# Kernel optimization log

Hardware: AMD Instinct MI355X
Metric: run time of the kernel (lower is better)

The kernel has to match this reference:

```python
import jax, jax.numpy as jnp
import numpy as np

N = 100000
E = 1600000
C = 192      # in_channels
GH = 256     # grapher hidden
FH = 512     # ffn hidden
EPS = 1e-5


def _bn(x, gamma, beta):
    # BatchNorm1d, training-mode batch statistics over the node axis
    mean = jnp.mean(x, axis=0)
    var = jnp.var(x, axis=0)
    return (x - mean) * jax.lax.rsqrt(var + EPS) * gamma + beta


def setup_inputs() -> dict:
    key = jax.random.key(0)
    ks = jax.random.split(key, 12)
    s = 0.02
    inp = {
        "x": jax.random.normal(ks[0], (N, C), dtype=jnp.float32),
        "edge_index": jax.random.randint(ks[1], (2, E), 0, N, dtype=jnp.int64),
        # Grapher fc1
        "Wg1": jax.random.normal(ks[2], (C, GH), jnp.float32) * s,
        "bg1": jnp.zeros((GH,), jnp.float32),
        "gg1": jnp.ones((GH,), jnp.float32),
        "beg1": jnp.zeros((GH,), jnp.float32),
        # GraphConv (lin_rel has bias, lin_root no bias, per PyG)
        "Wrel": jax.random.normal(ks[3], (GH, GH), jnp.float32) * s,
        "brel": jnp.zeros((GH,), jnp.float32),
        "Wroot": jax.random.normal(ks[4], (GH, GH), jnp.float32) * s,
        # Grapher fc2
        "Wg2": jax.random.normal(ks[5], (GH, C), jnp.float32) * s,
        "bg2": jnp.zeros((C,), jnp.float32),
        "gg2": jnp.ones((C,), jnp.float32),
        "beg2": jnp.zeros((C,), jnp.float32),
        # FFN fc1
        "Wf1": jax.random.normal(ks[6], (C, FH), jnp.float32) * s,
        "bf1": jnp.zeros((FH,), jnp.float32),
        "gf1": jnp.ones((FH,), jnp.float32),
        "bef1": jnp.zeros((FH,), jnp.float32),
        # FFN fc2
        "Wf2": jax.random.normal(ks[7], (FH, C), jnp.float32) * s,
        "bf2": jnp.zeros((C,), jnp.float32),
        "gf2": jnp.ones((C,), jnp.float32),
        "bef2": jnp.zeros((C,), jnp.float32),
    }
    return inp


def reference(x, edge_index, Wg1, bg1, gg1, beg1, Wrel, brel, Wroot,
              Wg2, bg2, gg2, beg2, Wf1, bf1, gf1, bef1, Wf2, bf2, gf2, bef2):
    n = x.shape[0]
    src, dst = edge_index[0], edge_index[1]

    # ---- Grapher ----
    shortcut = x
    h = _bn(x @ Wg1 + bg1, gg1, beg1)                       # [N, GH]
    # GraphConv: sum-aggregate neighbor messages at target nodes
    agg = jax.ops.segment_sum(h[src], dst, num_segments=n)  # [N, GH]
    gc = agg @ Wrel + brel + h @ Wroot
    h = jax.nn.gelu(gc, approximate=False)
    h = _bn(h @ Wg2 + bg2, gg2, beg2)                       # [N, C]
    x = h + shortcut

    # ---- FFN ----
    shortcut = x
    h = jax.nn.gelu(_bn(x @ Wf1 + bf1, gf1, bef1), approximate=False)
    h = _bn(h @ Wf2 + bf2, gf2, bef2)
    return h + shortcut
```

## Files before the change

kernel.cpp:

```cpp
#include <hip/hip_runtime.h>
#include <math.h>

typedef __bf16 bf16x8 __attribute__((ext_vector_type(8)));
typedef float  floatx4 __attribute__((ext_vector_type(4)));

__device__ inline float bf_lo(unsigned u){ return __uint_as_float(u << 16); }
__device__ inline float bf_hi(unsigned u){ return __uint_as_float(u & 0xffff0000u); }
__device__ inline unsigned short f2bf_u(float f){
    unsigned u = __float_as_uint(f);
    return (unsigned short)((u + 0x7fffu + ((u >> 16) & 1u)) >> 16);
}
__device__ inline unsigned pack2(float a, float b){
    return (unsigned)f2bf_u(a) | ((unsigned)f2bf_u(b) << 16);
}
__device__ inline float gelu_f(float v){
    return 0.5f * v * (1.f + erff(v * 0.70710678118654752f));
}
__device__ inline void gload_lds16(const void* g, void* l){
    __builtin_amdgcn_global_load_lds(
        (const __attribute__((address_space(1))) unsigned int*)g,
        (__attribute__((address_space(3))) unsigned int*)l, 16, 0, 0);
}

__global__ void zero_k(int* __restrict__ p, int n){
    int i = blockIdx.x * 256 + threadIdx.x;
    if (i < n) p[i] = 0;
}

__global__ void xcast_k(const float* __restrict__ x, unsigned short* __restrict__ xb, long n8){
    long i = (long)blockIdx.x * 256 + threadIdx.x;
    if (i < n8){
        const float4* p = (const float4*)(x + i * 8);
        float4 a = p[0], b = p[1];
        uint4 o;
        o.x = pack2(a.x, a.y); o.y = pack2(a.z, a.w);
        o.z = pack2(b.x, b.y); o.w = pack2(b.z, b.w);
        *(uint4*)(xb + i * 8) = o;
    }
}

__global__ void wprep_k(const float* __restrict__ W, unsigned short* __restrict__ Wt,
                        int K, int Ncols, int ostride, int ooffs){
    int idx = blockIdx.x * 256 + threadIdx.x;
    if (idx < K * Ncols){
        int k = idx / Ncols, n = idx - k * Ncols;
        Wt[(size_t)n * ostride + ooffs + k] = f2bf_u(W[idx]);
    }
}

__global__ void mkbn_k(const float* __restrict__ gsum, const float* __restrict__ gsq,
                       const float* __restrict__ gamma, const float* __restrict__ beta,
                       const float* __restrict__ brel,
                       float* __restrict__ scv, float* __restrict__ shv,
                       float* __restrict__ bias2, float* __restrict__ rvec,
                       int C_, float invN){
    int c = blockIdx.x * 256 + threadIdx.x;
    if (c < C_){
        float mean = gsum[c] * invN;
        float var  = gsq[c] * invN - mean * mean;
        float sc   = gamma[c] * rsqrtf(var + 1e-5f);
        scv[c] = sc;
        shv[c] = beta[c] - mean * sc;
        bias2[c] = brel[c];
        rvec[c]  = 0.f;
    }
}

__global__ void wscale_k(unsigned short* __restrict__ wt, const float* __restrict__ scv, int total){
    int i = blockIdx.x * 256 + threadIdx.x;
    if (i < total){
        float v = __uint_as_float(((unsigned)wt[i]) << 16);
        wt[i] = f2bf_u(v * scv[i & 255]);
    }
}

__global__ void biasrr_k(const float* __restrict__ Wrel, const float* __restrict__ Wroot,
                         const float* __restrict__ shv,
                         float* __restrict__ bias2, float* __restrict__ rvec){
    int m = threadIdx.x;
    int k0 = blockIdx.x * 32;
    float b2 = 0.f, rv = 0.f;
    for (int k = k0; k < k0 + 32; ++k){
        float s = shv[k];
        rv = fmaf(s, Wrel[k * 256 + m], rv);
        b2 = fmaf(s, Wroot[k * 256 + m], b2);
    }
    atomicAdd(&bias2[m], b2);
    atomicAdd(&rvec[m],  rv);
}

#define RBSH 9
#define RB   512
#define PCH  8192

__global__ __launch_bounds__(256)
void bhist_k(const int* __restrict__ dst, int* __restrict__ bcnt, int E){
    __shared__ int h[256];
    for (int i = threadIdx.x; i < 256; i += 256) h[i] = 0;
    __syncthreads();
    for (long i = (long)blockIdx.x * 256 + threadIdx.x; i < E; i += (long)gridDim.x * 256)
        atomicAdd(&h[dst[i] >> RBSH], 1);
    __syncthreads();
    int v = h[threadIdx.x];
    if (v) atomicAdd(&bcnt[threadIdx.x * 16], v);
}

__global__ void bscan_k(const int* __restrict__ bcnt, int* __restrict__ bbase,
                        int* __restrict__ bcur, int nbuk, int E){
    __shared__ int s[256];
    const int t = threadIdx.x;
    int v = (t < nbuk) ? bcnt[t * 16] : 0;
    s[t] = v; __syncthreads();
    for (int d = 1; d < 256; d <<= 1){
        int tt = (t >= d) ? s[t - d] : 0;
        __syncthreads();
        s[t] += tt;
        __syncthreads();
    }
    int excl = s[t] - v;
    if (t < nbuk){ bbase[t] = excl; bcur[t * 16] = excl; }
    if (t == 0) bbase[nbuk] = E;
}

__global__ __launch_bounds__(512)
void bpart_k(const int* __restrict__ src, const int* __restrict__ dst,
             int* __restrict__ bcur, int2* __restrict__ pairs, int E){
    __shared__ int h[256];
    __shared__ int s[256];
    __shared__ int cur[256];
    const int t = threadIdx.x;
    const int base = blockIdx.x * PCH;
    const int cnt = min(PCH, E - base);
    if (t < 256) h[t] = 0;
    __syncthreads();
    for (int i = t; i < cnt; i += 512)
        atomicAdd(&h[dst[base + i] >> RBSH], 1);
    __syncthreads();
    if (t < 256) s[t] = h[t];
    __syncthreads();
    for (int d = 1; d < 256; d <<= 1){
        int tt = 0;
        if (t < 256 && t >= d) tt = s[t - d];
        __syncthreads();
        if (t < 256) s[t] += tt;
        __syncthreads();
    }
    if (t < 256){
        int myc = h[t];
        int g = 0;
        if (myc) g = atomicAdd(&bcur[t * 16], myc);
        cur[t] = g;
    }
    __syncthreads();
    for (int i = t; i < cnt; i += 512){
        int d = dst[base + i];
        int b = d >> RBSH;
        int r = atomicAdd(&cur[b], 1);
        pairs[r] = make_int2(src[base + i], d);
    }
}

__global__ __launch_bounds__(1024)
void bbuild_k(const int2* __restrict__ pairs, const int* __restrict__ bbase,
              int* __restrict__ offsets, int* __restrict__ esrc, int N, int E){
    __shared__ int h[RB];
    __shared__ int s[RB];
    const int b = blockIdx.x;
    const int t = threadIdx.x;
    const int p0 = bbase[b], p1 = bbase[b + 1];
    if (t < RB) h[t] = 0;
    __syncthreads();
    for (int i = p0 + t; i < p1; i += 1024)
        atomicAdd(&h[pairs[i].y & (RB - 1)], 1);
    __syncthreads();
    int v = 0;
    if (t < RB){ v = h[t]; s[t] = v; }
    __syncthreads();
    for (int d = 1; d < RB; d <<= 1){
        int tt = 0;
        if (t < RB && t >= d) tt = s[t - d];
        __syncthreads();
        if (t < RB) s[t] += tt;
        __syncthreads();
    }
    if (t < RB){
        int node = (b << RBSH) + t;
        int excl = p0 + s[t] - v;
        if (node < N) offsets[node] = excl;
        h[t] = excl;
    }
    __syncthreads();
    for (int i = p0 + t; i < p1; i += 1024){
        int2 pr = pairs[i];
        int r = atomicAdd(&h[pr.y & (RB - 1)], 1);
        esrc[r] = pr.x;
    }
    if (b == 0 && t == 0) offsets[N] = E;
}

__global__ __launch_bounds__(256)
void agg_k(const unsigned short* __restrict__ hbn, const int* __restrict__ offsets,
           const int* __restrict__ esrc, unsigned short* __restrict__ aggout, int N){
    const int lane = threadIdx.x & 63;
    const int node = blockIdx.x * 4 + (threadIdx.x >> 6);
    if (node >= N) return;
    const int off  = offsets[node];
    const int end  = offsets[node + 1];
    const int half = lane >> 5;
    const int l32  = lane & 31;
    float a[8];
#pragma unroll
    for (int j = 0; j < 8; ++j) a[j] = 0.f;
    const unsigned short* hb = hbn + l32 * 8;
    for (int c = off; c < end; c += 64){
        const int e = c + lane;
        int sl = (e < end) ? esrc[e] : 0;
        const int cnt = min(64, end - c);
        for (int j = 0; j < cnt; j += 16){
            int   s[8];
            float m[8];
            uint4 u[8];
#pragma unroll
            for (int k = 0; k < 8; ++k){
                const int idx = j + 2 * k + half;
                s[k] = __shfl(sl, idx);
                m[k] = (idx < cnt) ? 1.f : 0.f;
            }
#pragma unroll
            for (int k = 0; k < 8; ++k)
                u[k] = *(const uint4*)(hb + (size_t)s[k] * 512);
#pragma unroll
            for (int k = 0; k < 8; ++k){
                a[0] = fmaf(m[k], bf_lo(u[k].x), a[0]);
                a[1] = fmaf(m[k], bf_hi(u[k].x), a[1]);
                a[2] = fmaf(m[k], bf_lo(u[k].y), a[2]);
                a[3] = fmaf(m[k], bf_hi(u[k].y), a[3]);
                a[4] = fmaf(m[k], bf_lo(u[k].z), a[4]);
                a[5] = fmaf(m[k], bf_hi(u[k].z), a[5]);
                a[6] = fmaf(m[k], bf_lo(u[k].w), a[6]);
                a[7] = fmaf(m[k], bf_hi(u[k].w), a[7]);
            }
        }
    }
#pragma unroll
    for (int j = 0; j < 8; ++j)
        a[j] += __shfl_xor(a[j], 32);
    if (half == 0){
        uint4 o;
        o.x = pack2(a[0], a[1]); o.y = pack2(a[2], a[3]);
        o.z = pack2(a[4], a[5]); o.w = pack2(a[6], a[7]);
        *(uint4*)(aggout + (size_t)node * 512 + l32 * 8) = o;
    }
}

template<int K, bool GELU_OUT, bool DEGBIAS, bool STATS>
__global__ __launch_bounds__(256)
void gemm3_k(const unsigned short* __restrict__ A, const unsigned short* __restrict__ Bt,
             const float* __restrict__ bias, unsigned short* __restrict__ Cp,
             long M, int NY, int ostride, int ooffs,
             const int* __restrict__ offs, const float* __restrict__ rvec,
             float* __restrict__ psum, float* __restrict__ psq){
    __shared__ unsigned short Xs[128 * 64];
    __shared__ unsigned short Ws[64 * 64];
    const int t    = threadIdx.x;
    const int lane = t & 63;
    const int w    = t >> 6;
    const int r16  = lane & 15;
    const int q4   = lane >> 4;

    const int nwg  = gridDim.x;
    const int orig = blockIdx.x;
    const int qq   = nwg >> 3, rr = nwg & 7;
    const int xcd  = orig & 7, kk = orig >> 3;
    const int wgid = (xcd < rr ? xcd * (qq + 1) : rr * (qq + 1) + (xcd - rr) * qq) + kk;
    const int xb   = wgid / NY;
    const int yb   = wgid - xb * NY;
    const long mbase = (long)xb * 128;
    const int  cb    = yb * 64;

    floatx4 acc[4][2];
#pragma unroll
    for (int ai = 0; ai < 4; ++ai)
#pragma unroll
        for (int bi = 0; bi < 2; ++bi) acc[ai][bi] = (floatx4)0.f;

    const int lrow = w * 8 + (lane >> 3);
    const int lk   = (lane & 7) * 8;
    const unsigned short* ga = A  + (size_t)(mbase + lrow) * K + lk;
    const unsigned short* gb = Bt + (size_t)(cb + lrow) * K + lk;
    unsigned short* lx = Xs + w * 512 + lane * 8;
    unsigned short* lw = Ws + w * 512 + lane * 8;

    for (int kt = 0; kt < K; kt += 64){
#pragma unroll
        for (int i = 0; i < 4; ++i)
            gload_lds16(ga + (size_t)i * 32 * K + kt, lx + i * 2048);
#pragma unroll
        for (int j = 0; j < 2; ++j)
            gload_lds16(gb + (size_t)j * 32 * K + kt, lw + j * 2048);
        asm volatile("s_waitcnt vmcnt(0)" ::: "memory");
        __syncthreads();
#pragma unroll
        for (int kc = 0; kc < 64; kc += 32){
            bf16x8 wf[4], xf[2];
#pragma unroll
            for (int ai = 0; ai < 4; ++ai)
                wf[ai] = *(const bf16x8*)(Ws + (ai * 16 + r16) * 64 + kc + q4 * 8);
#pragma unroll
            for (int bi = 0; bi < 2; ++bi)
                xf[bi] = *(const bf16x8*)(Xs + (w * 32 + bi * 16 + r16) * 64 + kc + q4 * 8);
#pragma unroll
            for (int ai = 0; ai < 4; ++ai)
#pragma unroll
                for (int bi = 0; bi < 2; ++bi)
                    acc[ai][bi] = __builtin_amdgcn_mfma_f32_16x16x32_bf16(
                        wf[ai], xf[bi], acc[ai][bi], 0, 0, 0);
        }
        __syncthreads();
    }

    float4 bv[4];
#pragma unroll
    for (int ai = 0; ai < 4; ++ai)
        bv[ai] = *(const float4*)(bias + cb + ai * 16 + q4 * 4);
    float4 rv[4];
    if constexpr (DEGBIAS){
#pragma unroll
        for (int ai = 0; ai < 4; ++ai)
            rv[ai] = *(const float4*)(rvec + cb + ai * 16 + q4 * 4);
    }
    float cs[4][4], cq[4][4];
    if constexpr (STATS){
#pragma unroll
        for (int ai = 0; ai < 4; ++ai)
#pragma unroll
            for (int j = 0; j < 4; ++j){ cs[ai][j] = 0.f; cq[ai][j] = 0.f; }
    }
#pragma unroll
    for (int bi = 0; bi < 2; ++bi){
        long node = mbase + w * 32 + bi * 16 + r16;
        const bool valid = node < M;
        float degf = 0.f;
        if constexpr (DEGBIAS){
            if (valid) degf = (float)(offs[node + 1] - offs[node]);
        }
        unsigned short* cp = Cp + (size_t)node * ostride + ooffs + cb;
#pragma unroll
        for (int ai = 0; ai < 4; ++ai){
            float v0 = acc[ai][bi][0] + bv[ai].x;
            float v1 = acc[ai][bi][1] + bv[ai].y;
            float v2 = acc[ai][bi][2] + bv[ai].z;
            float v3 = acc[ai][bi][3] + bv[ai].w;
            if constexpr (DEGBIAS){
                v0 = fmaf(degf, rv[ai].x, v0);
                v1 = fmaf(degf, rv[ai].y, v1);
                v2 = fmaf(degf, rv[ai].z, v2);
                v3 = fmaf(degf, rv[ai].w, v3);
            }
            if constexpr (STATS){
                float mm = valid ? 1.f : 0.f;
                cs[ai][0] += mm * v0; cq[ai][0] = fmaf(mm * v0, v0, cq[ai][0]);
                cs[ai][1] += mm * v1; cq[ai][1] = fmaf(mm * v1, v1, cq[ai][1]);
                cs[ai][2] += mm * v2; cq[ai][2] = fmaf(mm * v2, v2, cq[ai][2]);
                cs[ai][3] += mm * v3; cq[ai][3] = fmaf(mm * v3, v3, cq[ai][3]);
            }
            if constexpr (GELU_OUT){
                v0 = gelu_f(v0); v1 = gelu_f(v1); v2 = gelu_f(v2); v3 = gelu_f(v3);
            }
            if (valid){
                uint2 o; o.x = pack2(v0, v1); o.y = pack2(v2, v3);
                *(uint2*)(cp + ai * 16 + q4 * 4) = o;
            }
        }
    }

    if constexpr (STATS){
#pragma unroll
        for (int ai = 0; ai < 4; ++ai)
#pragma unroll
            for (int j = 0; j < 4; ++j){
#pragma unroll
                for (int m = 1; m < 16; m <<= 1){
                    cs[ai][j] += __shfl_xor(cs[ai][j], m);
                    cq[ai][j] += __shfl_xor(cq[ai][j], m);
                }
            }
        float* ssum = (float*)Xs;
        float* ssq  = ssum + 256;
        if (r16 == 0){
#pragma unroll
            for (int ai = 0; ai < 4; ++ai)
#pragma unroll
                for (int j = 0; j < 4; ++j){
                    ssum[w * 64 + ai * 16 + q4 * 4 + j] = cs[ai][j];
                    ssq [w * 64 + ai * 16 + q4 * 4 + j] = cq[ai][j];
                }
        }
        __syncthreads();
        if (t < 64){
            float s = 0.f, q = 0.f;
#pragma unroll
            for (int ww = 0; ww < 4; ++ww){ s += ssum[ww * 64 + t]; q += ssq[ww * 64 + t]; }
            const int nc = NY * 64;
            psum[(size_t)xb * nc + cb + t] = s;
            psq [(size_t)xb * nc + cb + t] = q;
        }
    }
}

__global__ void colreduce_k(const float* __restrict__ ps, const float* __restrict__ pq,
                            float* __restrict__ gsum, float* __restrict__ gsq,
                            int ncols, int nxb){
    __shared__ float ss[256], sq_[256];
    const int c = blockIdx.x;
    float s = 0.f, q = 0.f;
    for (int i = threadIdx.x; i < nxb; i += 256){
        s += ps[(size_t)i * ncols + c];
        q += pq[(size_t)i * ncols + c];
    }
    ss[threadIdx.x] = s; sq_[threadIdx.x] = q;
    __syncthreads();
    for (int d = 128; d > 0; d >>= 1){
        if (threadIdx.x < d){
            ss[threadIdx.x]  += ss[threadIdx.x + d];
            sq_[threadIdx.x] += sq_[threadIdx.x + d];
        }
        __syncthreads();
    }
    if (threadIdx.x == 0){ gsum[c] = ss[0]; gsq[c] = sq_[0]; }
}

template<int NCOLS, bool GELU_OUT, bool RES, bool RES_F32, bool OUT_F32>
__global__ __launch_bounds__(256)
void bn_apply_k(const unsigned short* __restrict__ in, void* __restrict__ outv,
                const void* __restrict__ resv,
                const float* __restrict__ gsum, const float* __restrict__ gsq,
                const float* __restrict__ gamma, const float* __restrict__ beta,
                long nrows, int ostride, int ooffs, float invN){
    __shared__ float s_scale[NCOLS], s_shift[NCOLS];
    for (int c = threadIdx.x; c < NCOLS; c += 256){
        float mean = gsum[c] * invN;
        float var  = gsq[c] * invN - mean * mean;
        float sc   = gamma[c] * rsqrtf(var + 1e-5f);
        s_scale[c] = sc;
        s_shift[c] = beta[c] - mean * sc;
    }
    __syncthreads();
    long i8 = ((long)blockIdx.x * 256 + threadIdx.x) * 8;
    if (i8 >= nrows * (long)NCOLS) return;
    long row  = i8 / NCOLS;
    int  col0 = (int)(i8 - row * NCOLS);
    uint4 u = *(const uint4*)(in + i8);
    float v[8];
    v[0] = bf_lo(u.x); v[1] = bf_hi(u.x); v[2] = bf_lo(u.y); v[3] = bf_hi(u.y);
    v[4] = bf_lo(u.z); v[5] = bf_hi(u.z); v[6] = bf_lo(u.w); v[7] = bf_hi(u.w);
#pragma unroll
    for (int j = 0; j < 8; ++j){
        v[j] = v[j] * s_scale[col0 + j] + s_shift[col0 + j];
        if constexpr (GELU_OUT) v[j] = gelu_f(v[j]);
    }
    if constexpr (RES){
        if constexpr (RES_F32){
            const float4* rp = (const float4*)((const float*)resv + i8);
            float4 r0 = rp[0], r1 = rp[1];
            v[0] += r0.x; v[1] += r0.y; v[2] += r0.z; v[3] += r0.w;
            v[4] += r1.x; v[5] += r1.y; v[6] += r1.z; v[7] += r1.w;
        } else {
            uint4 r = *(const uint4*)((const unsigned short*)resv + i8);
            v[0] += bf_lo(r.x); v[1] += bf_hi(r.x); v[2] += bf_lo(r.y); v[3] += bf_hi(r.y);
            v[4] += bf_lo(r.z); v[5] += bf_hi(r.z); v[6] += bf_lo(r.w); v[7] += bf_hi(r.w);
        }
    }
    long opos = row * ostride + ooffs + col0;
    if constexpr (OUT_F32){
        float4* op = (float4*)((float*)outv + opos);
        op[0] = make_float4(v[0], v[1], v[2], v[3]);
        op[1] = make_float4(v[4], v[5], v[6], v[7]);
    } else {
        uint4 o;
        o.x = pack2(v[0], v[1]); o.y = pack2(v[2], v[3]);
        o.z = pack2(v[4], v[5]); o.w = pack2(v[6], v[7]);
        *(uint4*)((unsigned short*)outv + opos) = o;
    }
}

extern "C" void kernel_launch(void* const* d_in, const int* in_sizes, int n_in,
                              void* d_out, int out_size, void* d_ws, size_t ws_size,
                              hipStream_t stream){
    const int C = 192, GH = 256, FH = 512;
    const float* x    = (const float*)d_in[0];
    const int*   ei   = (const int*)d_in[1];
    const float* Wg1  = (const float*)d_in[2];
    const float* bg1  = (const float*)d_in[3];
    const float* gg1  = (const float*)d_in[4];
    const float* beg1 = (const float*)d_in[5];
    const float* Wrel = (const float*)d_in[6];
    const float* brel = (const float*)d_in[7];
    const float* Wroot= (const float*)d_in[8];
    const float* Wg2  = (const float*)d_in[9];
    const float* bg2  = (const float*)d_in[10];
    const float* gg2  = (const float*)d_in[11];
    const float* beg2 = (const float*)d_in[12];
    const float* Wf1  = (const float*)d_in[13];
    const float* bf1  = (const float*)d_in[14];
    const float* gf1  = (const float*)d_in[15];
    const float* bef1 = (const float*)d_in[16];
    const float* Wf2  = (const float*)d_in[17];
    const float* bf2  = (const float*)d_in[18];
    const float* gf2  = (const float*)d_in[19];
    const float* bef2 = (const float*)d_in[20];

    const int N = in_sizes[0] / C;
    const int E = in_sizes[1] / 2;
    const int* e_src = ei;
    const int* e_dst = ei + E;

    char* wp = (char*)d_ws;
    auto carve = [&](size_t bytes) -> void* {
        void* p = (void*)wp; wp += (bytes + 255) & ~(size_t)255; return p;
    };
    unsigned short* wt_g1 = (unsigned short*)carve((size_t)GH * C * 2);
    unsigned short* wt_rr = (unsigned short*)carve((size_t)GH * 512 * 2);
    unsigned short* wt_g2 = (unsigned short*)carve((size_t)C * GH * 2);
    unsigned short* wt_f1 = (unsigned short*)carve((size_t)FH * C * 2);
    unsigned short* wt_f2 = (unsigned short*)carve((size_t)C * FH * 2);
    float* stats = (float*)carve(2 * (size_t)(GH + C + FH + C) * 4);
    float* sum1 = stats;        float* sq1 = sum1 + GH;
    float* sum2 = sq1 + GH;     float* sq2 = sum2 + C;
    float* sum3 = sq2 + C;      float* sq3 = sum3 + FH;
    float* sum4 = sq3 + FH;     float* sq4 = sum4 + C;
    float* scv   = (float*)carve(256 * 4);
    float* shv   = (float*)carve(256 * 4);
    float* bias2 = (float*)carve(256 * 4);
    float* rvec  = (float*)carve(256 * 4);
    const int GB = (N + 127) / 128;
    float* psum = (float*)carve((size_t)GB * 512 * 4);
    float* psq  = (float*)carve((size_t)GB * 512 * 4);
    unsigned short* buf0  = (unsigned short*)carve((size_t)N * 512 * 2);
    unsigned short* bufAG = (unsigned short*)carve((size_t)N * 512 * 2);
    int* offsets = (int*)carve((size_t)(N + 1) * 4);
    int* esrc    = (int*)carve((size_t)E * 4);
    int* bcnt    = (int*)carve((size_t)256 * 16 * 4);
    int* bbase   = (int*)carve((size_t)257 * 4);
    int* bcur    = (int*)carve((size_t)256 * 16 * 4);
    int2* pairs = (int2*)buf0;
    unsigned short* x_bf = buf0;
    unsigned short* g    = buf0;
    unsigned short* f1   = buf0;
    unsigned short* AG   = bufAG;
    unsigned short* h2   = bufAG;
    unsigned short* h4   = bufAG + (size_t)N * C;
    (void)ws_size; (void)n_in; (void)out_size;

    const float invN = 1.0f / (float)N;
    const int nbuk = (N + RB - 1) >> RBSH;

    wprep_k<<<(C * GH + 255) / 256, 256, 0, stream>>>(Wg1, wt_g1, C, GH, C, 0);
    wprep_k<<<(GH * GH + 255) / 256, 256, 0, stream>>>(Wrel, wt_rr, GH, GH, 512, 0);
    wprep_k<<<(GH * GH + 255) / 256, 256, 0, stream>>>(Wroot, wt_rr, GH, GH, 512, GH);
    wprep_k<<<(GH * C + 255) / 256, 256, 0, stream>>>(Wg2, wt_g2, GH, C, GH, 0);
    wprep_k<<<(C * FH + 255) / 256, 256, 0, stream>>>(Wf1, wt_f1, C, FH, C, 0);
    wprep_k<<<(FH * C + 255) / 256, 256, 0, stream>>>(Wf2, wt_f2, FH, C, FH, 0);

    zero_k<<<(256 * 16 + 255) / 256, 256, 0, stream>>>(bcnt, 256 * 16);

    bhist_k<<<1024, 256, 0, stream>>>(e_dst, bcnt, E);
    bscan_k<<<1, 256, 0, stream>>>(bcnt, bbase, bcur, nbuk, E);
    bpart_k<<<(E + PCH - 1) / PCH, 512, 0, stream>>>(e_src, e_dst, bcur, pairs, E);
    bbuild_k<<<nbuk, 1024, 0, stream>>>(pairs, bbase, offsets, esrc, N, E);

    xcast_k<<<(int)(((size_t)N * C / 8 + 255) / 256), 256, 0, stream>>>(x, x_bf, (long)N * C / 8);

    gemm3_k<192, false, false, true><<<GB * (GH / 64), 256, 0, stream>>>(
        x_bf, wt_g1, bg1, AG, N, GH / 64, 512, 256, nullptr, nullptr, psum, psq);
    colreduce_k<<<GH, 256, 0, stream>>>(psum, psq, sum1, sq1, GH, GB);
    mkbn_k<<<1, 256, 0, stream>>>(sum1, sq1, gg1, beg1, brel, scv, shv, bias2, rvec, GH, invN);
    wscale_k<<<(GH * 512 + 255) / 256, 256, 0, stream>>>(wt_rr, scv, GH * 512);
    biasrr_k<<<8, 256, 0, stream>>>(Wrel, Wroot, shv, bias2, rvec);
    agg_k<<<(N + 3) / 4, 256, 0, stream>>>(AG + 256, offsets, esrc, AG, N);
    gemm3_k<512, true, true, false><<<GB * (GH / 64), 256, 0, stream>>>(
        AG, wt_rr, bias2, g, N, GH / 64, GH, 0, offsets, rvec, nullptr, nullptr);
    gemm3_k<256, false, false, true><<<GB * (C / 64), 256, 0, stream>>>(
        g, wt_g2, bg2, h2, N, C / 64, C, 0, nullptr, nullptr, psum, psq);
    colreduce_k<<<C, 256, 0, stream>>>(psum, psq, sum2, sq2, C, GB);
    bn_apply_k<192, false, true, true, false><<<(int)(((size_t)N * C / 8 + 255) / 256), 256, 0, stream>>>(
        h2, h2, x, sum2, sq2, gg2, beg2, N, 192, 0, invN);

    gemm3_k<192, false, false, true><<<GB * (FH / 64), 256, 0, stream>>>(
        h2, wt_f1, bf1, f1, N, FH / 64, FH, 0, nullptr, nullptr, psum, psq);
    colreduce_k<<<FH, 256, 0, stream>>>(psum, psq, sum3, sq3, FH, GB);
    bn_apply_k<512, true, false, false, false><<<(int)(((size_t)N * FH / 8 + 255) / 256), 256, 0, stream>>>(
        f1, f1, nullptr, sum3, sq3, gf1, bef1, N, 512, 0, invN);
    gemm3_k<512, false, false, true><<<GB * (C / 64), 256, 0, stream>>>(
        f1, wt_f2, bf2, h4, N, C / 64, C, 0, nullptr, nullptr, psum, psq);
    colreduce_k<<<C, 256, 0, stream>>>(psum, psq, sum4, sq4, C, GB);
    bn_apply_k<192, false, true, false, true><<<(int)(((size_t)N * C / 8 + 255) / 256), 256, 0, stream>>>(
        h4, d_out, h2, sum4, sq4, gf2, bef2, N, 192, 0, invN);
}
```

Baseline: 768.8 us.

## Fuse x bf16 cast and FFN BN+GELU into GEMM A-tile loads

```diff
diff --git a/kernel.cpp b/kernel.cpp
--- a/kernel.cpp
+++ b/kernel.cpp
@@ -25,18 +25,6 @@
 __global__ void zero_k(int* __restrict__ p, int n){
     int i = blockIdx.x * 256 + threadIdx.x;
     if (i < n) p[i] = 0;
-}
-
-__global__ void xcast_k(const float* __restrict__ x, unsigned short* __restrict__ xb, long n8){
-    long i = (long)blockIdx.x * 256 + threadIdx.x;
-    if (i < n8){
-        const float4* p = (const float4*)(x + i * 8);
-        float4 a = p[0], b = p[1];
-        uint4 o;
-        o.x = pack2(a.x, a.y); o.y = pack2(a.z, a.w);
-        o.z = pack2(b.x, b.y); o.w = pack2(b.z, b.w);
-        *(uint4*)(xb + i * 8) = o;
-    }
 }
 
 __global__ void wprep_k(const float* __restrict__ W, unsigned short* __restrict__ Wt,
@@ -66,6 +54,19 @@
     }
 }
 
+__global__ void mksc_k(const float* __restrict__ gsum, const float* __restrict__ gsq,
+                       const float* __restrict__ gamma, const float* __restrict__ beta,
+                       float* __restrict__ scv, float* __restrict__ shv, int C_, float invN){
+    int c = blockIdx.x * 256 + threadIdx.x;
+    if (c < C_){
+        float mean = gsum[c] * invN;
+        float var  = gsq[c] * invN - mean * mean;
+        float sc   = gamma[c] * rsqrtf(var + 1e-5f);
+        scv[c] = sc;
+        shv[c] = beta[c] - mean * sc;
+    }
+}
+
 __global__ void wscale_k(unsigned short* __restrict__ wt, const float* __restrict__ scv, int total){
     int i = blockIdx.x * 256 + threadIdx.x;
     if (i < total){
@@ -253,13 +254,14 @@
     }
 }
 
-template<int K, bool GELU_OUT, bool DEGBIAS, bool STATS>
+template<int K, bool GELU_OUT, bool DEGBIAS, bool STATS, int AMODE>
 __global__ __launch_bounds__(256)
-void gemm3_k(const unsigned short* __restrict__ A, const unsigned short* __restrict__ Bt,
+void gemm3_k(const void* __restrict__ Ap, const unsigned short* __restrict__ Bt,
              const float* __restrict__ bias, unsigned short* __restrict__ Cp,
              long M, int NY, int ostride, int ooffs,
              const int* __restrict__ offs, const float* __restrict__ rvec,
-             float* __restrict__ psum, float* __restrict__ psq){
+             float* __restrict__ psum, float* __restrict__ psq,
+             const float* __restrict__ scA, const float* __restrict__ shA){
     __shared__ unsigned short Xs[128 * 64];
     __shared__ unsigned short Ws[64 * 64];
     const int t    = threadIdx.x;
@@ -286,15 +288,53 @@
 
     const int lrow = w * 8 + (lane >> 3);
     const int lk   = (lane & 7) * 8;
-    const unsigned short* ga = A  + (size_t)(mbase + lrow) * K + lk;
-    const unsigned short* gb = Bt + (size_t)(cb + lrow) * K + lk;
+    const unsigned short* gaH = (const unsigned short*)Ap + (size_t)(mbase + lrow) * K + lk;
+    const unsigned short* gb  = Bt + (size_t)(cb + lrow) * K + lk;
     unsigned short* lx = Xs + w * 512 + lane * 8;
     unsigned short* lw = Ws + w * 512 + lane * 8;
 
     for (int kt = 0; kt < K; kt += 64){
-#pragma unroll
-        for (int i = 0; i < 4; ++i)
-            gload_lds16(ga + (size_t)i * 32 * K + kt, lx + i * 2048);
+        if constexpr (AMODE == 0){
+#pragma unroll
+            for (int i = 0; i < 4; ++i)
+                gload_lds16(gaH + (size_t)i * 32 * K + kt, lx + i * 2048);
+        } else if constexpr (AMODE == 1){
+#pragma unroll
+            for (int i = 0; i < 4; ++i){
+                long r = mbase + i * 32 + lrow;
+                if (r >= M) r = M - 1;
+                const float* p = (const float*)Ap + r * K + lk + kt;
+                float4 a = *(const float4*)p;
+                float4 b = *(const float4*)(p + 4);
+                uint4 o;
+                o.x = pack2(a.x, a.y); o.y = pack2(a.z, a.w);
+                o.z = pack2(b.x, b.y); o.w = pack2(b.z, b.w);
+                *(uint4*)(lx + i * 2048) = o;
+            }
+        } else {
+            float4 s0 = *(const float4*)(scA + kt + lk);
+            float4 s1 = *(const float4*)(scA + kt + lk + 4);
+            float4 h0 = *(const float4*)(shA + kt + lk);
+            float4 h1 = *(const float4*)(shA + kt + lk + 4);
+#pragma unroll
+            for (int i = 0; i < 4; ++i){
+                uint4 u = *(const uint4*)(gaH + (size_t)i * 32 * K + kt);
+                float v0 = fmaf(bf_lo(u.x), s0.x, h0.x);
+                float v1 = fmaf(bf_hi(u.x), s0.y, h0.y);
+                float v2 = fmaf(bf_lo(u.y), s0.z, h0.z);
+                float v3 = fmaf(bf_hi(u.y), s0.w, h0.w);
+                float v4 = fmaf(bf_lo(u.z), s1.x, h1.x);
+                float v5 = fmaf(bf_hi(u.z), s1.y, h1.y);
+                float v6 = fmaf(bf_lo(u.w), s1.z, h1.z);
+                float v7 = fmaf(bf_hi(u.w), s1.w, h1.w);
+                v0 = gelu_f(v0); v1 = gelu_f(v1); v2 = gelu_f(v2); v3 = gelu_f(v3);
+                v4 = gelu_f(v4); v5 = gelu_f(v5); v6 = gelu_f(v6); v7 = gelu_f(v7);
+                uint4 o;
+                o.x = pack2(v0, v1); o.y = pack2(v2, v3);
+                o.z = pack2(v4, v5); o.w = pack2(v6, v7);
+                *(uint4*)(lx + i * 2048) = o;
+            }
+        }
 #pragma unroll
         for (int j = 0; j < 2; ++j)
             gload_lds16(gb + (size_t)j * 32 * K + kt, lw + j * 2048);
@@ -533,6 +573,8 @@
     float* shv   = (float*)carve(256 * 4);
     float* bias2 = (float*)carve(256 * 4);
     float* rvec  = (float*)carve(256 * 4);
+    float* sc3   = (float*)carve(512 * 4);
+    float* sh3   = (float*)carve(512 * 4);
     const int GB = (N + 127) / 128;
     float* psum = (float*)carve((size_t)GB * 512 * 4);
     float* psq  = (float*)carve((size_t)GB * 512 * 4);
@@ -544,7 +586,6 @@
     int* bbase   = (int*)carve((size_t)257 * 4);
     int* bcur    = (int*)carve((size_t)256 * 16 * 4);
     int2* pairs = (int2*)buf0;
-    unsigned short* x_bf = buf0;
     unsigned short* g    = buf0;
     unsigned short* f1   = buf0;
     unsigned short* AG   = bufAG;
@@ -569,30 +610,27 @@
     bpart_k<<<(E + PCH - 1) / PCH, 512, 0, stream>>>(e_src, e_dst, bcur, pairs, E);
     bbuild_k<<<nbuk, 1024, 0, stream>>>(pairs, bbase, offsets, esrc, N, E);
 
-    xcast_k<<<(int)(((size_t)N * C / 8 + 255) / 256), 256, 0, stream>>>(x, x_bf, (long)N * C / 8);
-
-    gemm3_k<192, false, false, true><<<GB * (GH / 64), 256, 0, stream>>>(
-        x_bf, wt_g1, bg1, AG, N, GH / 64, 512, 256, nullptr, nullptr, psum, psq);
+    gemm3_k<192, false, false, true, 1><<<GB * (GH / 64), 256, 0, stream>>>(
+        x, wt_g1, bg1, AG, N, GH / 64, 512, 256, nullptr, nullptr, psum, psq, nullptr, nullptr);
     colreduce_k<<<GH, 256, 0, stream>>>(psum, psq, sum1, sq1, GH, GB);
     mkbn_k<<<1, 256, 0, stream>>>(sum1, sq1, gg1, beg1, brel, scv, shv, bias2, rvec, GH, invN);
     wscale_k<<<(GH * 512 + 255) / 256, 256, 0, stream>>>(wt_rr, scv, GH * 512);
     biasrr_k<<<8, 256, 0, stream>>>(Wrel, Wroot, shv, bias2, rvec);
     agg_k<<<(N + 3) / 4, 256, 0, stream>>>(AG + 256, offsets, esrc, AG, N);
-    gemm3_k<512, true, true, false><<<GB * (GH / 64), 256, 0, stream>>>(
-        AG, wt_rr, bias2, g, N, GH / 64, GH, 0, offsets, rvec, nullptr, nullptr);
-    gemm3_k<256, false, false, true><<<GB * (C / 64), 256, 0, stream>>>(
-        g, wt_g2, bg2, h2, N, C / 64, C, 0, nullptr, nullptr, psum, psq);
+    gemm3_k<512, true, true, false, 0><<<GB * (GH / 64), 256, 0, stream>>>(
+        AG, wt_rr, bias2, g, N, GH / 64, GH, 0, offsets, rvec, nullptr, nullptr, nullptr, nullptr);
+    gemm3_k<256, false, false, true, 0><<<GB * (C / 64), 256, 0, stream>>>(
+        g, wt_g2, bg2, h2, N, C / 64, C, 0, nullptr, nullptr, psum, psq, nullptr, nullptr);
     colreduce_k<<<C, 256, 0, stream>>>(psum, psq, sum2, sq2, C, GB);
     bn_apply_k<192, false, true, true, false><<<(int)(((size_t)N * C / 8 + 255) / 256), 256, 0, stream>>>(
         h2, h2, x, sum2, sq2, gg2, beg2, N, 192, 0, invN);
 
-    gemm3_k<192, false, false, true><<<GB * (FH / 64), 256, 0, stream>>>(
-        h2, wt_f1, bf1, f1, N, FH / 64, FH, 0, nullptr, nullptr, psum, psq);
+    gemm3_k<192, false, false, true, 0><<<GB * (FH / 64), 256, 0, stream>>>(
+        h2, wt_f1, bf1, f1, N, FH / 64, FH, 0, nullptr, nullptr, psum, psq, nullptr, nullptr);
     colreduce_k<<<FH, 256, 0, stream>>>(psum, psq, sum3, sq3, FH, GB);
-    bn_apply_k<512, true, false, false, false><<<(int)(((size_t)N * FH / 8 + 255) / 256), 256, 0, stream>>>(
-        f1, f1, nullptr, sum3, sq3, gf1, bef1, N, 512, 0, invN);
-    gemm3_k<512, false, false, true><<<GB * (C / 64), 256, 0, stream>>>(
-        f1, wt_f2, bf2, h4, N, C / 64, C, 0, nullptr, nullptr, psum, psq);
+    mksc_k<<<2, 256, 0, stream>>>(sum3, sq3, gf1, bef1, sc3, sh3, FH, invN);
+    gemm3_k<512, false, false, true, 2><<<GB * (C / 64), 256, 0, stream>>>(
+        f1, wt_f2, bf2, h4, N, C / 64, C, 0, nullptr, nullptr, psum, psq, sc3, sh3);
     colreduce_k<<<C, 256, 0, stream>>>(psum, psq, sum4, sq4, C, GB);
     bn_apply_k<192, false, true, false, true><<<(int)(((size_t)N * C / 8 + 255) / 256), 256, 0, stream>>>(
         h4, d_out, h2, sum4, sq4, gf2, bef2, N, 192, 0, invN);
```

New measurement: 813.0 us. 1.06x slower.
